# Optimization experiments

Hardware: AMD Instinct MI355X
Metric: run time of the kernel (lower is better)

Reference implementation:

```python
import jax, jax.numpy as jnp
import numpy as np

N_QUERIES = 33_554_432  # 32M query points (128 MB fp32)
N_KNOTS = 1024          # interpolation table size


def setup_inputs() -> dict:
    key = jax.random.key(0)
    k1, k2, k3 = jax.random.split(key, 3)
    # queries spread slightly beyond the knot range to exercise clamping branches
    x = jax.random.uniform(k1, (N_QUERIES,), dtype=jnp.float32, minval=-0.1, maxval=1.1)
    # unsorted knots (module sorts them in __init__; reference sorts too)
    x_points = jax.random.uniform(k2, (N_KNOTS,), dtype=jnp.float32)
    y_points = jax.random.normal(k3, (N_KNOTS,), dtype=jnp.float32)
    return {"x": x, "x_points": x_points, "y_points": y_points}


def reference(x, x_points, y_points):
    # __init__: sort knots by x, permute y accordingly
    order = jnp.argsort(x_points)
    xp = x_points[order]
    yp = y_points[order]
    n = xp.shape[0]
    # torch.searchsorted default (right=False) == side='left'
    idx = jnp.searchsorted(xp, x, side="left")  # [N], int
    # interior lerp uses (idx-1, idx); clip so gathers are in-range
    hi = jnp.clip(idx, 1, n - 1)
    lo = hi - 1
    x1, x2 = xp[lo], xp[hi]
    y1, y2 = yp[lo], yp[hi]
    interp = y1 + (x - x1) * (y2 - y1) / (x2 - x1)
    # boundary clamps: idx==0 -> y[0]; idx>=n -> y[-1]
    out = jnp.where(idx == 0, yp[0], jnp.where(idx >= n, yp[-1], interp))
    return out
```

## Files before the change

### kernel.cpp

```cpp
#include <hip/hip_runtime.h>
#include <math.h>

#define NK 1024
#define NB 4096

#define WS_SXP   0
#define WS_META  1032
#define WS_QUAD  1040
#define WS_TAB   5136
#define WS_FTAB  7184

typedef float f4v __attribute__((ext_vector_type(4)));

__device__ __forceinline__ int bucket_of(float x, float lo, float scale) {
    float t = __fmul_rn(__fsub_rn(x, lo), scale);
    int b = (int)t;
    b = b < 0 ? 0 : b;
    b = b > (NB - 1) ? (NB - 1) : b;
    return b;
}

__global__ __launch_bounds__(1024) void setup_kernel(
        const float* __restrict__ xp_in, const float* __restrict__ yp_in,
        float* __restrict__ wsf)
{
    __shared__ unsigned long long keys[NK];
    __shared__ float sx[NK + 8];
    __shared__ float sy[NK];
    __shared__ float slp[NK];
    __shared__ unsigned short tabs[NB];

    const int t = threadIdx.x;

    float xv = xp_in[t];
    unsigned int fb  = __float_as_uint(xv);
    unsigned int k32 = (fb & 0x80000000u) ? ~fb : (fb | 0x80000000u);
    keys[t] = ((unsigned long long)k32 << 10) | (unsigned int)t;
    __syncthreads();

    for (int k = 2; k <= NK; k <<= 1) {
        for (int j = k >> 1; j > 0; j >>= 1) {
            int ixj = t ^ j;
            if (ixj > t) {
                unsigned long long a = keys[t], b = keys[ixj];
                bool up = ((t & k) == 0);
                if ((a > b) == up) { keys[t] = b; keys[ixj] = a; }
            }
            __syncthreads();
        }
    }

    unsigned long long key = keys[t];
    unsigned int s32 = (unsigned int)(key >> 10);
    unsigned int xb  = (s32 & 0x80000000u) ? (s32 ^ 0x80000000u) : ~s32;
    float xs = __uint_as_float(xb);
    sx[t] = xs;
    sy[t] = yp_in[(int)(key & (NK - 1))];
    if (t < 8) sx[NK + t] = INFINITY;
    __syncthreads();

    const float lo  = sx[0];
    const float xpN = sx[NK - 1];
    float range = xpN - lo;
    const float scale     = (range > 0.0f) ? ((float)NB / range) : 0.0f;
    const float inv_scale = range * (1.0f / (float)NB);

    slp[t] = (t < NK - 1) ? (sy[t + 1] - sy[t]) / (sx[t + 1] - sx[t]) : 0.0f;
    __syncthreads();

    for (int k = 0; k < 4; ++k) {
        int b = 4 * t + k;
        int loi = 0, hii = NK;
        while (loi < hii) {
            int mid = (loi + hii) >> 1;
            if (bucket_of(sx[mid], lo, scale) < b) loi = mid + 1; else hii = mid;
        }
        tabs[b] = (unsigned short)loi;
    }
    __syncthreads();

    float2*         ftabg = (float2*)(wsf + WS_FTAB);
    unsigned short* tabg  = (unsigned short*)(wsf + WS_TAB);
    for (int k = 0; k < 4; ++k) {
        int b   = 4 * t + k;
        int ib  = tabs[b];
        int ib1 = (b == NB - 1) ? NK : tabs[b + 1];
        int interior = ib1 - ib - (b == 0 ? 1 : 0) - (b == NB - 1 ? 1 : 0);
        int hi = ib < 1 ? 1 : (ib > NK - 1 ? NK - 1 : ib);
        float2 e;
        if (interior > 0) {
            e.x = __uint_as_float(0x7fc00000u);
            e.y = 0.0f;
        } else {
            float a  = slp[hi - 1];
            float bl = __fmaf_rn((float)b, inv_scale, lo);
            e.x = a;
            e.y = __fmaf_rn(bl - sx[hi - 1], a, sy[hi - 1]);
        }
        ftabg[b] = e;
        tabg[b]  = (unsigned short)ib;
    }

    wsf[t] = sx[t];
    if (t < 8) wsf[NK + t] = INFINITY;
    float4* qg = (float4*)(wsf + WS_QUAD);
    qg[t] = make_float4(sx[t], sy[t], slp[t], 0.0f);
    if (t == 0) {
        wsf[WS_META + 0] = lo;
        wsf[WS_META + 1] = inv_scale;
        wsf[WS_META + 2] = scale;
        wsf[WS_META + 3] = sy[0];
        wsf[WS_META + 4] = sy[NK - 1];
        wsf[WS_META + 5] = xpN;
    }
}

__device__ __forceinline__ float interp_one(
        float x, const float2* __restrict__ ftab,
        const float* __restrict__ gsxp, const float4* __restrict__ gquads,
        const unsigned short* __restrict__ gtab,
        float lo, float inv_scale, float scale, float xpN, float yp0, float ypN)
{
    int b = bucket_of(x, lo, scale);
    float2 e = ftab[b];
    float bl  = __fmaf_rn((float)b, inv_scale, lo);
    float res = __fmaf_rn(x - bl, e.x, e.y);
    if (__builtin_isnan(e.x) && x > lo && x <= xpN) {
        int j = gtab[b];
        for (;;) {
            float s0 = gsxp[j], s1 = gsxp[j + 1], s2 = gsxp[j + 2], s3 = gsxp[j + 3];
            int c = (s0 < x) + (s1 < x) + (s2 < x) + (s3 < x);
            j += c;
            if (c < 4) break;
        }
        int hi = j < 1 ? 1 : (j > NK - 1 ? NK - 1 : j);
        float4 qd = gquads[hi - 1];
        res = __fmaf_rn(x - qd.x, qd.z, qd.y);
    }
    res = (x <= lo)  ? yp0 : res;
    res = (x >  xpN) ? ypN : res;
    return res;
}

__global__ __launch_bounds__(512, 8) void interp_kernel(
        const f4v* __restrict__ xq, f4v* __restrict__ out,
        const float* __restrict__ wsf, int n4)
{
    __shared__ __align__(16) float2 ftab[NB];
    const int t = threadIdx.x;
    {
        const f4v* src = (const f4v*)(wsf + WS_FTAB);
        f4v*       dst = (f4v*)ftab;
        #pragma unroll
        for (int i = 0; i < 4; ++i) dst[t + 512 * i] = src[t + 512 * i];
    }
    const float lo        = wsf[WS_META + 0];
    const float inv_scale = wsf[WS_META + 1];
    const float scale     = wsf[WS_META + 2];
    const float yp0       = wsf[WS_META + 3];
    const float ypN       = wsf[WS_META + 4];
    const float xpN       = wsf[WS_META + 5];
    const float*          gsxp   = wsf + WS_SXP;
    const float4*         gquads = (const float4*)(wsf + WS_QUAD);
    const unsigned short* gtab   = (const unsigned short*)(wsf + WS_TAB);
    __syncthreads();

    int q = blockIdx.x * 512 + t;
    const int stride = gridDim.x * 512;
    for (; q + stride < n4; q += 2 * stride) {
        f4v xa = __builtin_nontemporal_load(&xq[q]);
        f4v xb = __builtin_nontemporal_load(&xq[q + stride]);
        f4v ra, rb;
        ra.x = interp_one(xa.x, ftab, gsxp, gquads, gtab, lo, inv_scale, scale, xpN, yp0, ypN);
        ra.y = interp_one(xa.y, ftab, gsxp, gquads, gtab, lo, inv_scale, scale, xpN, yp0, ypN);
        ra.z = interp_one(xa.z, ftab, gsxp, gquads, gtab, lo, inv_scale, scale, xpN, yp0, ypN);
        ra.w = interp_one(xa.w, ftab, gsxp, gquads, gtab, lo, inv_scale, scale, xpN, yp0, ypN);
        __builtin_nontemporal_store(ra, &out[q]);
        rb.x = interp_one(xb.x, ftab, gsxp, gquads, gtab, lo, inv_scale, scale, xpN, yp0, ypN);
        rb.y = interp_one(xb.y, ftab, gsxp, gquads, gtab, lo, inv_scale, scale, xpN, yp0, ypN);
        rb.z = interp_one(xb.z, ftab, gsxp, gquads, gtab, lo, inv_scale, scale, xpN, yp0, ypN);
        rb.w = interp_one(xb.w, ftab, gsxp, gquads, gtab, lo, inv_scale, scale, xpN, yp0, ypN);
        __builtin_nontemporal_store(rb, &out[q + stride]);
    }
    for (; q < n4; q += stride) {
        f4v xa = __builtin_nontemporal_load(&xq[q]);
        f4v ra;
        ra.x = interp_one(xa.x, ftab, gsxp, gquads, gtab, lo, inv_scale, scale, xpN, yp0, ypN);
        ra.y = interp_one(xa.y, ftab, gsxp, gquads, gtab, lo, inv_scale, scale, xpN, yp0, ypN);
        ra.z = interp_one(xa.z, ftab, gsxp, gquads, gtab, lo, inv_scale, scale, xpN, yp0, ypN);
        ra.w = interp_one(xa.w, ftab, gsxp, gquads, gtab, lo, inv_scale, scale, xpN, yp0, ypN);
        __builtin_nontemporal_store(ra, &out[q]);
    }
}

extern "C" void kernel_launch(void* const* d_in, const int* in_sizes, int n_in,
                              void* d_out, int out_size, void* d_ws, size_t ws_size,
                              hipStream_t stream)
{
    const float* x  = (const float*)d_in[0];
    const float* xp = (const float*)d_in[1];
    const float* yp = (const float*)d_in[2];
    float* out = (float*)d_out;
    float* wsf = (float*)d_ws;

    setup_kernel<<<1, 1024, 0, stream>>>(xp, yp, wsf);

    const int n4 = out_size / 4;
    interp_kernel<<<1024, 512, 0, stream>>>((const f4v*)x, (f4v*)out, wsf, n4);
}
```

Baseline: 284.5 us.

## Split setup into shuffle-based sort and multi-block table build, cache knots in LDS

```diff
diff --git a/kernel.cpp b/kernel.cpp
--- a/kernel.cpp
+++ b/kernel.cpp
@@ -7,8 +7,7 @@
 #define WS_SXP   0
 #define WS_META  1032
 #define WS_QUAD  1040
-#define WS_TAB   5136
-#define WS_FTAB  7184
+#define WS_FTAB  5136
 
 typedef float f4v __attribute__((ext_vector_type(4)));
 
@@ -20,105 +19,120 @@
     return b;
 }
 
-__global__ __launch_bounds__(1024) void setup_kernel(
+__global__ __launch_bounds__(1024) void setup_sort(
         const float* __restrict__ xp_in, const float* __restrict__ yp_in,
         float* __restrict__ wsf)
 {
-    __shared__ unsigned long long keys[NK];
-    __shared__ float sx[NK + 8];
-    __shared__ float sy[NK];
-    __shared__ float slp[NK];
-    __shared__ unsigned short tabs[NB];
+    __shared__ unsigned long long kl[NK];
+    __shared__ float sxs[NK];
+    __shared__ float sys[NK];
 
     const int t = threadIdx.x;
 
     float xv = xp_in[t];
     unsigned int fb  = __float_as_uint(xv);
     unsigned int k32 = (fb & 0x80000000u) ? ~fb : (fb | 0x80000000u);
-    keys[t] = ((unsigned long long)k32 << 10) | (unsigned int)t;
-    __syncthreads();
+    unsigned long long key = ((unsigned long long)k32 << 10) | (unsigned int)t;
 
     for (int k = 2; k <= NK; k <<= 1) {
-        for (int j = k >> 1; j > 0; j >>= 1) {
-            int ixj = t ^ j;
-            if (ixj > t) {
-                unsigned long long a = keys[t], b = keys[ixj];
-                bool up = ((t & k) == 0);
-                if ((a > b) == up) { keys[t] = b; keys[ixj] = a; }
-            }
+        const bool dir = ((t & k) == 0);
+        for (int j = k >> 1; j >= 64; j >>= 1) {
+            kl[t] = key;
             __syncthreads();
+            unsigned long long p = kl[t ^ j];
+            __syncthreads();
+            bool lower = ((t & j) == 0);
+            bool wmin  = (dir == lower);
+            unsigned long long mn = key < p ? key : p;
+            unsigned long long mx = key < p ? p : key;
+            key = wmin ? mn : mx;
         }
-    }
-
-    unsigned long long key = keys[t];
-    unsigned int s32 = (unsigned int)(key >> 10);
-    unsigned int xb  = (s32 & 0x80000000u) ? (s32 ^ 0x80000000u) : ~s32;
+        for (int j = ((k >> 1) >= 64 ? 32 : (k >> 1)); j >= 1; j >>= 1) {
+            unsigned long long p = __shfl_xor(key, j, 64);
+            bool lower = ((t & j) == 0);
+            bool wmin  = (dir == lower);
+            unsigned long long mn = key < p ? key : p;
+            unsigned long long mx = key < p ? p : key;
+            key = wmin ? mn : mx;
+        }
+    }
+
+    unsigned int idx0 = (unsigned int)(key & (NK - 1));
+    unsigned int s32  = (unsigned int)(key >> 10);
+    unsigned int xb   = (s32 & 0x80000000u) ? (s32 ^ 0x80000000u) : ~s32;
     float xs = __uint_as_float(xb);
-    sx[t] = xs;
-    sy[t] = yp_in[(int)(key & (NK - 1))];
-    if (t < 8) sx[NK + t] = INFINITY;
-    __syncthreads();
-
-    const float lo  = sx[0];
-    const float xpN = sx[NK - 1];
-    float range = xpN - lo;
-    const float scale     = (range > 0.0f) ? ((float)NB / range) : 0.0f;
-    const float inv_scale = range * (1.0f / (float)NB);
-
-    slp[t] = (t < NK - 1) ? (sy[t + 1] - sy[t]) / (sx[t + 1] - sx[t]) : 0.0f;
-    __syncthreads();
-
-    for (int k = 0; k < 4; ++k) {
-        int b = 4 * t + k;
+    float ys = yp_in[idx0];
+    sxs[t] = xs; sys[t] = ys;
+    __syncthreads();
+
+    float xn = (t < NK - 1) ? sxs[t + 1] : xs;
+    float yn = (t < NK - 1) ? sys[t + 1] : ys;
+    float slope = (t < NK - 1) ? (yn - ys) / (xn - xs) : 0.0f;
+
+    wsf[WS_SXP + t] = xs;
+    if (t < 8) wsf[WS_SXP + NK + t] = INFINITY;
+    ((float4*)(wsf + WS_QUAD))[t] = make_float4(xs, ys, slope, 0.0f);
+    if (t == 0) {
+        float lo  = sxs[0];
+        float xpN = sxs[NK - 1];
+        float range = xpN - lo;
+        wsf[WS_META + 0] = lo;
+        wsf[WS_META + 1] = range * (1.0f / (float)NB);
+        wsf[WS_META + 2] = (range > 0.0f) ? ((float)NB / range) : 0.0f;
+        wsf[WS_META + 3] = sys[0];
+        wsf[WS_META + 4] = sys[NK - 1];
+        wsf[WS_META + 5] = xpN;
+    }
+}
+
+__global__ __launch_bounds__(256) void setup_tables(float* __restrict__ wsf)
+{
+    __shared__ float sxp_s[NK];
+    __shared__ int   lb[257];
+    __shared__ float meta[6];
+
+    const int tid = threadIdx.x;
+    for (int i = tid; i < NK; i += 256) sxp_s[i] = wsf[WS_SXP + i];
+    if (tid < 6) meta[tid] = wsf[WS_META + tid];
+    __syncthreads();
+
+    const float lo = meta[0], inv_scale = meta[1], scale = meta[2];
+    const int base = blockIdx.x * 256;
+
+    auto lbf = [&](int b) -> int {
         int loi = 0, hii = NK;
         while (loi < hii) {
             int mid = (loi + hii) >> 1;
-            if (bucket_of(sx[mid], lo, scale) < b) loi = mid + 1; else hii = mid;
+            if (bucket_of(sxp_s[mid], lo, scale) < b) loi = mid + 1; else hii = mid;
         }
-        tabs[b] = (unsigned short)loi;
-    }
-    __syncthreads();
-
-    float2*         ftabg = (float2*)(wsf + WS_FTAB);
-    unsigned short* tabg  = (unsigned short*)(wsf + WS_TAB);
-    for (int k = 0; k < 4; ++k) {
-        int b   = 4 * t + k;
-        int ib  = tabs[b];
-        int ib1 = (b == NB - 1) ? NK : tabs[b + 1];
-        int interior = ib1 - ib - (b == 0 ? 1 : 0) - (b == NB - 1 ? 1 : 0);
+        return loi;
+    };
+    lb[tid] = lbf(base + tid);
+    if (tid == 0) lb[256] = (base + 256 >= NB) ? NK : lbf(base + 256);
+    __syncthreads();
+
+    const int b   = base + tid;
+    const int ib  = lb[tid];
+    const int ib1 = lb[tid + 1];
+    const int interior = ib1 - ib - (b == 0 ? 1 : 0) - (b == NB - 1 ? 1 : 0);
+
+    float2 e;
+    if (interior > 0) {
+        e.x = __uint_as_float(0x7fc00000u);
+        e.y = __uint_as_float((unsigned int)ib);
+    } else {
         int hi = ib < 1 ? 1 : (ib > NK - 1 ? NK - 1 : ib);
-        float2 e;
-        if (interior > 0) {
-            e.x = __uint_as_float(0x7fc00000u);
-            e.y = 0.0f;
-        } else {
-            float a  = slp[hi - 1];
-            float bl = __fmaf_rn((float)b, inv_scale, lo);
-            e.x = a;
-            e.y = __fmaf_rn(bl - sx[hi - 1], a, sy[hi - 1]);
-        }
-        ftabg[b] = e;
-        tabg[b]  = (unsigned short)ib;
-    }
-
-    wsf[t] = sx[t];
-    if (t < 8) wsf[NK + t] = INFINITY;
-    float4* qg = (float4*)(wsf + WS_QUAD);
-    qg[t] = make_float4(sx[t], sy[t], slp[t], 0.0f);
-    if (t == 0) {
-        wsf[WS_META + 0] = lo;
-        wsf[WS_META + 1] = inv_scale;
-        wsf[WS_META + 2] = scale;
-        wsf[WS_META + 3] = sy[0];
-        wsf[WS_META + 4] = sy[NK - 1];
-        wsf[WS_META + 5] = xpN;
-    }
+        float4 qd = ((const float4*)(wsf + WS_QUAD))[hi - 1];
+        float bl = __fmaf_rn((float)b, inv_scale, lo);
+        e.x = qd.z;
+        e.y = __fmaf_rn(bl - qd.x, qd.z, qd.y);
+    }
+    ((float2*)(wsf + WS_FTAB))[b] = e;
 }
 
 __device__ __forceinline__ float interp_one(
-        float x, const float2* __restrict__ ftab,
-        const float* __restrict__ gsxp, const float4* __restrict__ gquads,
-        const unsigned short* __restrict__ gtab,
+        float x, const float2* __restrict__ ftab, const float* __restrict__ sxp,
+        const float4* __restrict__ gquads,
         float lo, float inv_scale, float scale, float xpN, float yp0, float ypN)
 {
     int b = bucket_of(x, lo, scale);
@@ -126,14 +140,9 @@
     float bl  = __fmaf_rn((float)b, inv_scale, lo);
     float res = __fmaf_rn(x - bl, e.x, e.y);
     if (__builtin_isnan(e.x) && x > lo && x <= xpN) {
-        int j = gtab[b];
-        for (;;) {
-            float s0 = gsxp[j], s1 = gsxp[j + 1], s2 = gsxp[j + 2], s3 = gsxp[j + 3];
-            int c = (s0 < x) + (s1 < x) + (s2 < x) + (s3 < x);
-            j += c;
-            if (c < 4) break;
-        }
-        int hi = j < 1 ? 1 : (j > NK - 1 ? NK - 1 : j);
+        int j = (int)__float_as_uint(e.y);
+        while (sxp[j] < x) ++j;
+        int hi = j < 1 ? 1 : j;
         float4 qd = gquads[hi - 1];
         res = __fmaf_rn(x - qd.x, qd.z, qd.y);
     }
@@ -147,12 +156,14 @@
         const float* __restrict__ wsf, int n4)
 {
     __shared__ __align__(16) float2 ftab[NB];
+    __shared__ float sxp_s[NK + 8];
     const int t = threadIdx.x;
     {
         const f4v* src = (const f4v*)(wsf + WS_FTAB);
         f4v*       dst = (f4v*)ftab;
         #pragma unroll
         for (int i = 0; i < 4; ++i) dst[t + 512 * i] = src[t + 512 * i];
+        for (int i = t; i < NK + 8; i += 512) sxp_s[i] = wsf[WS_SXP + i];
     }
     const float lo        = wsf[WS_META + 0];
     const float inv_scale = wsf[WS_META + 1];
@@ -160,35 +171,33 @@
     const float yp0       = wsf[WS_META + 3];
     const float ypN       = wsf[WS_META + 4];
     const float xpN       = wsf[WS_META + 5];
-    const float*          gsxp   = wsf + WS_SXP;
-    const float4*         gquads = (const float4*)(wsf + WS_QUAD);
-    const unsigned short* gtab   = (const unsigned short*)(wsf + WS_TAB);
+    const float4* gquads  = (const float4*)(wsf + WS_QUAD);
     __syncthreads();
 
     int q = blockIdx.x * 512 + t;
     const int stride = gridDim.x * 512;
     for (; q + stride < n4; q += 2 * stride) {
-        f4v xa = __builtin_nontemporal_load(&xq[q]);
-        f4v xb = __builtin_nontemporal_load(&xq[q + stride]);
+        f4v xa = xq[q];
+        f4v xb = xq[q + stride];
         f4v ra, rb;
-        ra.x = interp_one(xa.x, ftab, gsxp, gquads, gtab, lo, inv_scale, scale, xpN, yp0, ypN);
-        ra.y = interp_one(xa.y, ftab, gsxp, gquads, gtab, lo, inv_scale, scale, xpN, yp0, ypN);
-        ra.z = interp_one(xa.z, ftab, gsxp, gquads, gtab, lo, inv_scale, scale, xpN, yp0, ypN);
-        ra.w = interp_one(xa.w, ftab, gsxp, gquads, gtab, lo, inv_scale, scale, xpN, yp0, ypN);
+        ra.x = interp_one(xa.x, ftab, sxp_s, gquads, lo, inv_scale, scale, xpN, yp0, ypN);
+        ra.y = interp_one(xa.y, ftab, sxp_s, gquads, lo, inv_scale, scale, xpN, yp0, ypN);
+        ra.z = interp_one(xa.z, ftab, sxp_s, gquads, lo, inv_scale, scale, xpN, yp0, ypN);
+        ra.w = interp_one(xa.w, ftab, sxp_s, gquads, lo, inv_scale, scale, xpN, yp0, ypN);
+        rb.x = interp_one(xb.x, ftab, sxp_s, gquads, lo, inv_scale, scale, xpN, yp0, ypN);
+        rb.y = interp_one(xb.y, ftab, sxp_s, gquads, lo, inv_scale, scale, xpN, yp0, ypN);
+        rb.z = interp_one(xb.z, ftab, sxp_s, gquads, lo, inv_scale, scale, xpN, yp0, ypN);
+        rb.w = interp_one(xb.w, ftab, sxp_s, gquads, lo, inv_scale, scale, xpN, yp0, ypN);
         __builtin_nontemporal_store(ra, &out[q]);
-        rb.x = interp_one(xb.x, ftab, gsxp, gquads, gtab, lo, inv_scale, scale, xpN, yp0, ypN);
-        rb.y = interp_one(xb.y, ftab, gsxp, gquads, gtab, lo, inv_scale, scale, xpN, yp0, ypN);
-        rb.z = interp_one(xb.z, ftab, gsxp, gquads, gtab, lo, inv_scale, scale, xpN, yp0, ypN);
-        rb.w = interp_one(xb.w, ftab, gsxp, gquads, gtab, lo, inv_scale, scale, xpN, yp0, ypN);
         __builtin_nontemporal_store(rb, &out[q + stride]);
     }
     for (; q < n4; q += stride) {
-        f4v xa = __builtin_nontemporal_load(&xq[q]);
+        f4v xa = xq[q];
         f4v ra;
-        ra.x = interp_one(xa.x, ftab, gsxp, gquads, gtab, lo, inv_scale, scale, xpN, yp0, ypN);
-        ra.y = interp_one(xa.y, ftab, gsxp, gquads, gtab, lo, inv_scale, scale, xpN, yp0, ypN);
-        ra.z = interp_one(xa.z, ftab, gsxp, gquads, gtab, lo, inv_scale, scale, xpN, yp0, ypN);
-        ra.w = interp_one(xa.w, ftab, gsxp, gquads, gtab, lo, inv_scale, scale, xpN, yp0, ypN);
+        ra.x = interp_one(xa.x, ftab, sxp_s, gquads, lo, inv_scale, scale, xpN, yp0, ypN);
+        ra.y = interp_one(xa.y, ftab, sxp_s, gquads, lo, inv_scale, scale, xpN, yp0, ypN);
+        ra.z = interp_one(xa.z, ftab, sxp_s, gquads, lo, inv_scale, scale, xpN, yp0, ypN);
+        ra.w = interp_one(xa.w, ftab, sxp_s, gquads, lo, inv_scale, scale, xpN, yp0, ypN);
         __builtin_nontemporal_store(ra, &out[q]);
     }
 }
@@ -203,7 +212,8 @@
     float* out = (float*)d_out;
     float* wsf = (float*)d_ws;
 
-    setup_kernel<<<1, 1024, 0, stream>>>(xp, yp, wsf);
+    setup_sort<<<1, 1024, 0, stream>>>(xp, yp, wsf);
+    setup_tables<<<NB / 256, 256, 0, stream>>>(wsf);
 
     const int n4 = out_size / 4;
     interp_kernel<<<1024, 512, 0, stream>>>((const f4v*)x, (f4v*)out, wsf, n4);
```

After: 262.3 us. -7.8%, faster.
